# Performance work log

Measured on AMD Instinct MI355X. Metric: run time of the kernel, lower is better.

## Reference

```python
import jax, jax.numpy as jnp
import numpy as np

N = 50000      # nodes
E = 800000     # edges (avg degree 16)
H = 128        # hidden_nf
NORM_FACTOR = 100.0   # normalization_factor, aggregation 'sum'
NORM_CONST = 1.0      # norm_constant (effective_constant = max(1, 1.0))
EPS = 1e-8


def silu(v):
    return v * jax.nn.sigmoid(v)


def setup_inputs() -> dict:
    key = jax.random.key(0)
    ks = jax.random.split(key, 16)
    IN_E = 2 * H + 2  # edge MLP input: h[row] | h[col] | [radial, edge_attr]

    def w(k, shape, scale=0.05):
        return jax.random.normal(k, shape, dtype=jnp.float32) * scale

    return {
        "h": jax.random.normal(ks[0], (N, H), dtype=jnp.float32),
        "x": jax.random.normal(ks[1], (N, 3), dtype=jnp.float32),
        "edge_index": jax.random.randint(ks[2], (2, E), 0, N, dtype=jnp.int32),
        "edge_attr": jax.random.normal(ks[3], (E, 1), dtype=jnp.float32),
        "node_mask": jnp.ones((N, 1), dtype=jnp.float32),
        "edge_mask": jnp.ones((E, 1), dtype=jnp.float32),
        # 2 stacked GCL layers (identical shapes -> stacked on leading dim)
        "gcl_e_w1": w(ks[4], (2, IN_E, H)), "gcl_e_b1": jnp.zeros((2, H), jnp.float32),
        "gcl_e_w2": w(ks[5], (2, H, H)),    "gcl_e_b2": jnp.zeros((2, H), jnp.float32),
        "gcl_a_w":  w(ks[6], (2, H, 1)),    "gcl_a_b":  jnp.zeros((2, 1), jnp.float32),
        "gcl_n_w1": w(ks[7], (2, 2 * H, H)),"gcl_n_b1": jnp.zeros((2, H), jnp.float32),
        "gcl_n_w2": w(ks[8], (2, H, H)),    "gcl_n_b2": jnp.zeros((2, H), jnp.float32),
        # EquivariantUpdate coord MLP (last layer xavier gain 0.001 -> tiny, no bias)
        "c_w1": w(ks[9], (IN_E, H)), "c_b1": jnp.zeros((H,), jnp.float32),
        "c_w2": w(ks[10], (H, H)),   "c_b2": jnp.zeros((H,), jnp.float32),
        "c_w3": w(ks[11], (H, 1), 0.001),
    }


def reference(h, x, edge_index, edge_attr, node_mask, edge_mask,
              gcl_e_w1, gcl_e_b1, gcl_e_w2, gcl_e_b2, gcl_a_w, gcl_a_b,
              gcl_n_w1, gcl_n_b1, gcl_n_w2, gcl_n_b2,
              c_w1, c_b1, c_w2, c_b2, c_w3):
    row, col = edge_index[0], edge_index[1]
    n_nodes = h.shape[0]

    # coord2diff
    diff = x[row] - x[col]                                  # [E,3]
    radial = jnp.sum(diff * diff, axis=1, keepdims=True)    # [E,1]
    norm = jnp.sqrt(radial + EPS)
    coord_diff = diff / (norm + NORM_CONST)

    # edge_attr = cat([distances, edge_attr])  -> edge_feat_nf = 2
    ea = jnp.concatenate([radial, edge_attr], axis=1)       # [E,2]

    # n_layers=2 GCLs with attention
    for i in range(2):
        einp = jnp.concatenate([h[row], h[col], ea], axis=1)             # [E,258]
        mij = silu(silu(einp @ gcl_e_w1[i] + gcl_e_b1[i]) @ gcl_e_w2[i] + gcl_e_b2[i])
        att = jax.nn.sigmoid(mij @ gcl_a_w[i] + gcl_a_b[i])
        ef = mij * att * edge_mask                                       # [E,H]
        agg = jax.ops.segment_sum(ef, row, num_segments=n_nodes) / NORM_FACTOR
        ninp = jnp.concatenate([h, agg], axis=1)                         # [N,2H]
        h = h + (silu(ninp @ gcl_n_w1[i] + gcl_n_b1[i]) @ gcl_n_w2[i] + gcl_n_b2[i])
        h = h * node_mask

    # EquivariantUpdate (tanh=False, reflection_equiv=True -> no cross term)
    einp = jnp.concatenate([h[row], h[col], ea], axis=1)
    phi = silu(silu(einp @ c_w1 + c_b1) @ c_w2 + c_b2) @ c_w3            # [E,1]
    trans = coord_diff * phi * edge_mask                                 # [E,3]
    aggx = jax.ops.segment_sum(trans, row, num_segments=n_nodes) / NORM_FACTOR
    x = (x + aggx) * node_mask

    h = h * node_mask
    return (h, x)
```

## Files before the change

### kernel.cpp

```cpp
#include <hip/hip_runtime.h>
#include <hip/hip_bf16.h>
#include <math.h>
#include <string.h>

#define DEV __device__ __forceinline__

typedef __bf16 bf16;
typedef bf16 bf16x8 __attribute__((ext_vector_type(8)));
typedef bf16 bf16x2 __attribute__((ext_vector_type(2)));
typedef float f32x4 __attribute__((ext_vector_type(4)));
typedef unsigned int uint;

constexpr int N_NODES = 50000;
constexpr int N_EDGES = 800000;
constexpr int H = 128;
constexpr int NB_SCAN = (N_NODES + 255) / 256;

DEV float fsilu(float x) { return x / (1.f + __expf(-x)); }
DEV float fsigmoid(float x) { return 1.f / (1.f + __expf(-x)); }


__global__ void transpose_pad_kernel(bf16* __restrict__ dst, const float* __restrict__ src,
                                     int K, int Nf, int KP) {
    int idx = blockIdx.x * 256 + threadIdx.x;
    if (idx >= Nf * KP) return;
    int n = idx / KP, k = idx - n * KP;
    dst[idx] = (k < K) ? (bf16)src[k * Nf + n] : (bf16)0.f;
}

__global__ void h_init_kernel(const float* __restrict__ h, float* __restrict__ h_cur, int n) {
    int i = blockIdx.x * 256 + threadIdx.x;
    if (i < n) h_cur[i] = h[i];
}

__global__ void out_h_kernel(const float* __restrict__ h_cur, const float* __restrict__ nmask,
                             float* __restrict__ out) {
    int i = blockIdx.x * 256 + threadIdx.x;
    if (i < N_NODES * H) out[i] = h_cur[i] * nmask[i >> 7];
}


__global__ void count_kernel(const int* __restrict__ ei, int* __restrict__ deg) {
    int e = blockIdx.x * 256 + threadIdx.x;
    if (e < N_EDGES) atomicAdd(&deg[ei[e]], 1);
}

__global__ void scan1_kernel(const int* __restrict__ deg, int* __restrict__ off,
                             int* __restrict__ bsum) {
    __shared__ int s[256];
    int t = threadIdx.x, i = blockIdx.x * 256 + t;
    int v = (i < N_NODES) ? deg[i] : 0;
    s[t] = v;
    __syncthreads();
#pragma unroll
    for (int st = 1; st < 256; st <<= 1) {
        int x = (t >= st) ? s[t - st] : 0;
        __syncthreads();
        s[t] += x;
        __syncthreads();
    }
    if (i < N_NODES) off[i] = s[t] - v;
    if (t == 255) bsum[blockIdx.x] = s[255];
}

__global__ void scan2_kernel(int* __restrict__ bsum) {
    __shared__ int s[256];
    int t = threadIdx.x;
    int v = (t < NB_SCAN) ? bsum[t] : 0;
    s[t] = v;
    __syncthreads();
#pragma unroll
    for (int st = 1; st < 256; st <<= 1) {
        int x = (t >= st) ? s[t - st] : 0;
        __syncthreads();
        s[t] += x;
        __syncthreads();
    }
    if (t < NB_SCAN) bsum[t] = s[t] - v;
}

__global__ void scan3_kernel(int* __restrict__ off, const int* __restrict__ bsum) {
    int i = blockIdx.x * 256 + threadIdx.x;
    if (i >= N_NODES) return;
    off[i] += bsum[blockIdx.x];
}

__global__ void fill2_kernel(const int* __restrict__ ei, const float* __restrict__ eattr,
                             const float* __restrict__ emask, int* __restrict__ off,
                             uint* __restrict__ rc_pm, bf16* __restrict__ eaem_pm) {
    int e = blockIdx.x * 256 + threadIdx.x;
    if (e >= N_EDGES) return;
    int r = ei[e], c = ei[N_EDGES + e];
    int slot = atomicAdd(&off[r], 1);
    rc_pm[slot] = ((uint)r << 16) | (uint)c;
    eaem_pm[(size_t)slot * 2 + 0] = (bf16)eattr[e];
    eaem_pm[(size_t)slot * 2 + 1] = (bf16)emask[e];
}

__global__ __launch_bounds__(256, 2) void pq_kernel(
    const float* __restrict__ h_cur, const bf16* __restrict__ w1t,
    const float* __restrict__ b1, bf16* __restrict__ P, bf16* __restrict__ Q) {
    __shared__ __align__(16) bf16 hs[64 * 128];
    int t = threadIdx.x, lane = t & 63, wv = t >> 6;
    int lr = lane & 15, lg = lane >> 4;
    int nbase = blockIdx.x * 64;

    {
        int nl = t >> 2, q = t & 3;
        int node = nbase + nl;
        if (node < N_NODES) {
            const float4* hr = (const float4*)(h_cur + (size_t)node * H);
#pragma unroll
            for (int c = 0; c < 4; ++c) {
                float4 v0 = hr[q * 8 + c * 2];
                float4 v1 = hr[q * 8 + c * 2 + 1];
                bf16x8 o;
                o[0] = (bf16)v0.x; o[1] = (bf16)v0.y; o[2] = (bf16)v0.z; o[3] = (bf16)v0.w;
                o[4] = (bf16)v1.x; o[5] = (bf16)v1.y; o[6] = (bf16)v1.z; o[7] = (bf16)v1.w;
                int sl = (q * 4 + c) ^ (nl & 7);
                *(bf16x8*)(hs + nl * 128 + sl * 8) = o;
            }
        } else {
#pragma unroll
            for (int c = 0; c < 4; ++c) {
                int sl = (q * 4 + c) ^ (nl & 7);
                *(bf16x8*)(hs + nl * 128 + sl * 8) = (bf16x8)(bf16)0.f;
            }
        }
    }
    __syncthreads();

    f32x4 aP[4][2], aQ[4][2];
#pragma unroll
    for (int er = 0; er < 4; ++er)
#pragma unroll
        for (int j = 0; j < 2; ++j) { aP[er][j] = (f32x4)0.f; aQ[er][j] = (f32x4)0.f; }

    const bf16* bp0 = w1t + (size_t)((wv * 2 + 0) * 16 + lr) * 256 + lg * 8;
    const bf16* bp1 = w1t + (size_t)((wv * 2 + 1) * 16 + lr) * 256 + lg * 8;
#pragma unroll
    for (int kk = 0; kk < 4; ++kk) {
        bf16x8 a[4];
#pragma unroll
        for (int er = 0; er < 4; ++er) {
            int sl = (kk * 4 + lg) ^ (lr & 7);
            a[er] = *(const bf16x8*)(hs + (er * 16 + lr) * 128 + sl * 8);
        }
        bf16x8 bP0 = *(const bf16x8*)(bp0 + kk * 32);
        bf16x8 bP1 = *(const bf16x8*)(bp1 + kk * 32);
        bf16x8 bQ0 = *(const bf16x8*)(bp0 + 128 + kk * 32);
        bf16x8 bQ1 = *(const bf16x8*)(bp1 + 128 + kk * 32);
#pragma unroll
        for (int er = 0; er < 4; ++er) {
            aP[er][0] = __builtin_amdgcn_mfma_f32_16x16x32_bf16(a[er], bP0, aP[er][0], 0, 0, 0);
            aP[er][1] = __builtin_amdgcn_mfma_f32_16x16x32_bf16(a[er], bP1, aP[er][1], 0, 0, 0);
            aQ[er][0] = __builtin_amdgcn_mfma_f32_16x16x32_bf16(a[er], bQ0, aQ[er][0], 0, 0, 0);
            aQ[er][1] = __builtin_amdgcn_mfma_f32_16x16x32_bf16(a[er], bQ1, aQ[er][1], 0, 0, 0);
        }
    }

    float bb0 = b1[(wv * 2 + 0) * 16 + lr];
    float bb1v = b1[(wv * 2 + 1) * 16 + lr];
#pragma unroll
    for (int er = 0; er < 4; ++er) {
#pragma unroll
        for (int j = 0; j < 2; ++j) {
            int feat = (wv * 2 + j) * 16 + lr;
            float bb = j ? bb1v : bb0;
#pragma unroll
            for (int r = 0; r < 4; ++r) {
                int node = nbase + er * 16 + lg * 4 + r;
                if (node < N_NODES) {
                    P[(size_t)node * H + feat] = (bf16)(aP[er][j][r] + bb);
                    Q[(size_t)node * H + feat] = (bf16)(aQ[er][j][r]);
                }
            }
        }
    }
}


__global__ __launch_bounds__(256) void gather_h_kernel(
    const bf16* __restrict__ ef, const int* __restrict__ off, bf16* __restrict__ agg_bf) {
    int t = threadIdx.x, lane = t & 63, wv = t >> 6;
    int n = blockIdx.x * 4 + wv;
    if (n >= N_NODES) return;
    int st = (n == 0) ? 0 : off[n - 1];
    int dg = off[n] - st;
    const bf16* bp = ef + (size_t)st * H + lane * 2;
    float s0 = 0.f, s1 = 0.f;
    for (int k = 0; k < dg; ++k) {
        uint v = *(const uint*)(bp + (size_t)k * H);
        s0 += __uint_as_float(v << 16);
        s1 += __uint_as_float(v & 0xffff0000u);
    }
    bf16x2 o;
    o[0] = (bf16)(s0 * 0.01f);
    o[1] = (bf16)(s1 * 0.01f);
    *(bf16x2*)(agg_bf + (size_t)n * H + lane * 2) = o;
}

__global__ __launch_bounds__(256) void gather_x_kernel(
    const float* __restrict__ trans, const int* __restrict__ off,
    const float* __restrict__ x, const float* __restrict__ nmask, float* __restrict__ outx) {
    int t = threadIdx.x, lane = t & 63, wv = t >> 6;
    int n = blockIdx.x * 4 + wv;
    if (n >= N_NODES) return;
    int st = (n == 0) ? 0 : off[n - 1];
    int dg = off[n] - st;
    float sx = 0.f, sy = 0.f, sz = 0.f;
    for (int k = lane; k < dg; k += 64) {
        const float* tp = trans + (size_t)(st + k) * 3;
        sx += tp[0];
        sy += tp[1];
        sz += tp[2];
    }
#pragma unroll
    for (int m = 1; m < 64; m <<= 1) {
        sx += __shfl_xor(sx, m);
        sy += __shfl_xor(sy, m);
        sz += __shfl_xor(sz, m);
    }
    if (lane == 0) {
        float nm = nmask[n];
        outx[n * 3 + 0] = (x[n * 3 + 0] + sx * 0.01f) * nm;
        outx[n * 3 + 1] = (x[n * 3 + 1] + sy * 0.01f) * nm;
        outx[n * 3 + 2] = (x[n * 3 + 2] + sz * 0.01f) * nm;
    }
}


template <int KCHUNKS, int ASTRIDE, int BSTRIDE>
DEV void wave_gemm(const bf16* A_lds, const bf16* __restrict__ Bt,
                   f32x4 (&acc)[4][2], int lr, int lg, int wv) {
#pragma unroll
    for (int kk = 0; kk < KCHUNKS; ++kk) {
        int ko = kk * 32 + lg * 8;
        bf16x8 a[4], b[2];
#pragma unroll
        for (int er = 0; er < 4; ++er)
            a[er] = *(const bf16x8*)(A_lds + (er * 16 + lr) * ASTRIDE + ko);
#pragma unroll
        for (int j = 0; j < 2; ++j)
            b[j] = *(const bf16x8*)(Bt + (size_t)((wv * 2 + j) * 16 + lr) * BSTRIDE + ko);
#pragma unroll
        for (int er = 0; er < 4; ++er)
#pragma unroll
            for (int j = 0; j < 2; ++j)
                acc[er][j] = __builtin_amdgcn_mfma_f32_16x16x32_bf16(a[er], b[j], acc[er][j], 0, 0, 0);
    }
}

DEV void epi_silu_store(const f32x4 (&acc)[4][2], const float* __restrict__ bias,
                        bf16* out_lds, int OSTRIDE, int lr, int lg, int wv) {
    float b0 = bias[(wv * 2 + 0) * 16 + lr];
    float b1 = bias[(wv * 2 + 1) * 16 + lr];
#pragma unroll
    for (int er = 0; er < 4; ++er) {
#pragma unroll
        for (int j = 0; j < 2; ++j) {
            float bb = j ? b1 : b0;
            int fcol = (wv * 2 + j) * 16 + lr;
#pragma unroll
            for (int r = 0; r < 4; ++r) {
                int rrow = er * 16 + lg * 4 + r;
                out_lds[rrow * OSTRIDE + fcol] = (bf16)fsilu(acc[er][j][r] + bb);
            }
        }
    }
}

DEV void epi_silu_store_swz(const f32x4 (&acc)[4][2], const float* __restrict__ bias,
                            bf16* out_lds, int lr, int lg, int wv) {
    float b0 = bias[(wv * 2 + 0) * 16 + lr];
    float b1 = bias[(wv * 2 + 1) * 16 + lr];
#pragma unroll
    for (int er = 0; er < 4; ++er) {
#pragma unroll
        for (int j = 0; j < 2; ++j) {
            float bb = j ? b1 : b0;
            int fcol = (wv * 2 + j) * 16 + lr;
#pragma unroll
            for (int r = 0; r < 4; ++r) {
                int rrow = er * 16 + lg * 4 + r;
                int sl = (fcol >> 3) ^ (rrow & 7);
                out_lds[rrow * 128 + sl * 8 + (fcol & 7)] = (bf16)fsilu(acc[er][j][r] + bb);
            }
        }
    }
}

template <int MODE>
__global__ __launch_bounds__(256, 4) void edge_kernel(
    const bf16* __restrict__ P, const bf16* __restrict__ Q,
    const uint* __restrict__ rc_pm, const bf16* __restrict__ eaem_pm,
    const float* __restrict__ xg,
    const float* __restrict__ w_r, const float* __restrict__ w_e,
    const bf16* __restrict__ w2t, const float* __restrict__ b2,
    const float* __restrict__ avec, const float* __restrict__ abias,
    bf16* __restrict__ efout, float* __restrict__ trans) {
    __shared__ __align__(16) bf16 AR[64 * 128];
    __shared__ __align__(16) bf16 AC[64 * 128];
    __shared__ __align__(16) float avec_l[128];

    int t = threadIdx.x, lane = t & 63, wv = t >> 6;
    int lr = lane & 15, lg = lane >> 4;
    int ebase = blockIdx.x * 64;
    int el = t >> 2, q = t & 3;

    {
        int rsub = lane >> 4;
        int slot = lane & 15;
#pragma unroll
        for (int u = 0; u < 4; ++u) {
            int r = wv * 16 + u * 4 + rsub;
            uint rc = rc_pm[ebase + r];
            int nr = (int)(rc >> 16);
            int nc = (int)(rc & 0xffffu);
            int sl = slot ^ (r & 7);
            const bf16* gpr = P + (size_t)nr * H + sl * 8;
            __builtin_amdgcn_global_load_lds(
                (const __attribute__((address_space(1))) void*)gpr,
                (__attribute__((address_space(3))) void*)&AR[(wv * 16 + u * 4) * 128],
                16, 0, 0);
            const bf16* gpc = Q + (size_t)nc * H + sl * 8;
            __builtin_amdgcn_global_load_lds(
                (const __attribute__((address_space(1))) void*)gpc,
                (__attribute__((address_space(3))) void*)&AC[(wv * 16 + u * 4) * 128],
                16, 0, 0);
        }
    }
    if (t >= 64 && t < 192) avec_l[t - 64] = avec[t - 64];

    uint rc = rc_pm[ebase + el];
    int rr = (int)(rc >> 16), cc = (int)(rc & 0xffffu);
    float dx = xg[rr * 3 + 0] - xg[cc * 3 + 0];
    float dy = xg[rr * 3 + 1] - xg[cc * 3 + 1];
    float dz = xg[rr * 3 + 2] - xg[cc * 3 + 2];
    float radial = dx * dx + dy * dy + dz * dz;
    uint eu = *(const uint*)(eaem_pm + (size_t)(ebase + el) * 2);
    bf16x2 ep = __builtin_bit_cast(bf16x2, eu);
    float eattr = (float)ep[0];
    float em = (float)ep[1];

    __syncthreads();

#pragma unroll
    for (int c = 0; c < 4; ++c) {
        int sl = (q * 4 + c) ^ (el & 7);
        bf16* ap = AR + el * 128 + sl * 8;
        bf16x8 pv = *(const bf16x8*)ap;
        bf16x8 qv = *(const bf16x8*)(AC + el * 128 + sl * 8);
        f32x4 wr0 = *(const f32x4*)(w_r + q * 32 + c * 8);
        f32x4 wr1 = *(const f32x4*)(w_r + q * 32 + c * 8 + 4);
        f32x4 we0 = *(const f32x4*)(w_e + q * 32 + c * 8);
        f32x4 we1 = *(const f32x4*)(w_e + q * 32 + c * 8 + 4);
        bf16x8 o;
#pragma unroll
        for (int jj = 0; jj < 4; ++jj) {
            float v = (float)pv[jj] + (float)qv[jj] + radial * wr0[jj] + eattr * we0[jj];
            o[jj] = (bf16)fsilu(v);
        }
#pragma unroll
        for (int jj = 0; jj < 4; ++jj) {
            float v = (float)pv[4 + jj] + (float)qv[4 + jj] + radial * wr1[jj] + eattr * we1[jj];
            o[4 + jj] = (bf16)fsilu(v);
        }
        *(bf16x8*)ap = o;
    }
    __syncthreads();

    f32x4 acc2[4][2];
#pragma unroll
    for (int er = 0; er < 4; ++er)
#pragma unroll
        for (int j = 0; j < 2; ++j) acc2[er][j] = (f32x4)0.f;
    {
        const bf16* cp0 = w2t + (size_t)((wv * 2 + 0) * 16 + lr) * 128 + lg * 8;
        const bf16* cp1 = w2t + (size_t)((wv * 2 + 1) * 16 + lr) * 128 + lg * 8;
#pragma unroll
        for (int kk = 0; kk < 4; ++kk) {
            bf16x8 a[4], b[2];
            b[0] = *(const bf16x8*)(cp0 + kk * 32);
            b[1] = *(const bf16x8*)(cp1 + kk * 32);
#pragma unroll
            for (int er = 0; er < 4; ++er) {
                int sl = (kk * 4 + lg) ^ (lr & 7);
                a[er] = *(const bf16x8*)(AR + (er * 16 + lr) * 128 + sl * 8);
            }
#pragma unroll
            for (int er = 0; er < 4; ++er)
#pragma unroll
                for (int j = 0; j < 2; ++j)
                    acc2[er][j] = __builtin_amdgcn_mfma_f32_16x16x32_bf16(a[er], b[j], acc2[er][j], 0, 0, 0);
        }
    }

    epi_silu_store_swz(acc2, b2, AC, lr, lg, wv);
    __syncthreads();

    float part = 0.f;
    bf16x8 mv[4];
#pragma unroll
    for (int c = 0; c < 4; ++c) {
        int sl = (q * 4 + c) ^ (el & 7);
        mv[c] = *(const bf16x8*)(AC + el * 128 + sl * 8);
        f32x4 av0 = *(const f32x4*)(avec_l + q * 32 + c * 8);
        f32x4 av1 = *(const f32x4*)(avec_l + q * 32 + c * 8 + 4);
#pragma unroll
        for (int jj = 0; jj < 4; ++jj) part += (float)mv[c][jj] * av0[jj];
#pragma unroll
        for (int jj = 0; jj < 4; ++jj) part += (float)mv[c][4 + jj] * av1[jj];
    }
    part += __shfl_xor(part, 1);
    part += __shfl_xor(part, 2);

    if (MODE == 0) {
        float att = fsigmoid(part + abias[0]);
        float scale = att * em;
        bf16* edst = efout + (size_t)(ebase + el) * H + q * 32;
#pragma unroll
        for (int c = 0; c < 4; ++c) {
            bf16x8 o;
#pragma unroll
            for (int jj = 0; jj < 8; ++jj) o[jj] = (bf16)((float)mv[c][jj] * scale);
            *(bf16x8*)(edst + c * 8) = o;
        }
    } else {
        if (q == 0) {
            float inv = 1.f / (sqrtf(radial + 1e-8f) + 1.f);
            float s = part * em * inv;
            int sI = ebase + el;
            trans[sI * 3 + 0] = dx * s;
            trans[sI * 3 + 1] = dy * s;
            trans[sI * 3 + 2] = dz * s;
        }
    }
}

__global__ __launch_bounds__(256, 2) void node_kernel(
    float* __restrict__ h_cur, const bf16* __restrict__ agg_bf,
    const bf16* __restrict__ w1t, const float* __restrict__ b1,
    const bf16* __restrict__ w2t, const float* __restrict__ b2,
    const float* __restrict__ nmask) {
    constexpr int SRN = 264;
    constexpr int TRN = 136;
    __shared__ __align__(16) bf16 ninp[64 * SRN];
    __shared__ __align__(16) bf16 t1[64 * TRN];

    int t = threadIdx.x, lane = t & 63, wv = t >> 6;
    int lr = lane & 15, lg = lane >> 4;
    int nbase = blockIdx.x * 64;

    {
        int nl = t >> 2, q = t & 3;
        int node = nbase + nl;
        bf16* dst = ninp + nl * SRN;
        if (node < N_NODES) {
            const float4* hr = (const float4*)(h_cur + (size_t)node * H);
            const bf16* ar = agg_bf + (size_t)node * H;
#pragma unroll
            for (int pp = 0; pp < 8; ++pp) {
                int ch = pp * 4 + q;
                float4 v = hr[ch];
                dst[ch * 4 + 0] = (bf16)v.x; dst[ch * 4 + 1] = (bf16)v.y;
                dst[ch * 4 + 2] = (bf16)v.z; dst[ch * 4 + 3] = (bf16)v.w;
            }
#pragma unroll
            for (int pp = 0; pp < 4; ++pp) {
                int ch = pp * 4 + q;
                *(bf16x8*)(dst + 128 + ch * 8) = *(const bf16x8*)(ar + ch * 8);
            }
        } else {
#pragma unroll
            for (int pp = 0; pp < 8; ++pp) {
                int ch = pp * 4 + q;
#pragma unroll
                for (int k = 0; k < 4; ++k) {
                    dst[ch * 4 + k] = (bf16)0.f;
                    dst[128 + ch * 4 + k] = (bf16)0.f;
                }
            }
        }
    }
    __syncthreads();

    f32x4 acc[4][2];
#pragma unroll
    for (int er = 0; er < 4; ++er)
#pragma unroll
        for (int j = 0; j < 2; ++j) acc[er][j] = (f32x4)0.f;
    wave_gemm<8, SRN, 256>(ninp, w1t, acc, lr, lg, wv);
    epi_silu_store(acc, b1, t1, TRN, lr, lg, wv);
    __syncthreads();

    f32x4 acc2[4][2];
#pragma unroll
    for (int er = 0; er < 4; ++er)
#pragma unroll
        for (int j = 0; j < 2; ++j) acc2[er][j] = (f32x4)0.f;
    wave_gemm<4, TRN, 128>(t1, w2t, acc2, lr, lg, wv);

    float bb0 = b2[(wv * 2 + 0) * 16 + lr];
    float bb1 = b2[(wv * 2 + 1) * 16 + lr];
#pragma unroll
    for (int er = 0; er < 4; ++er) {
#pragma unroll
        for (int j = 0; j < 2; ++j) {
            float bb = j ? bb1 : bb0;
            int feat = (wv * 2 + j) * 16 + lr;
#pragma unroll
            for (int r = 0; r < 4; ++r) {
                int node = nbase + er * 16 + lg * 4 + r;
                if (node < N_NODES) {
                    size_t idx = (size_t)node * H + feat;
                    float nm = nmask[node];
                    h_cur[idx] = (h_cur[idx] + acc2[er][j][r] + bb) * nm;
                }
            }
        }
    }
}

extern "C" void kernel_launch(void* const* d_in, const int* in_sizes, int n_in,
                              void* d_out, int out_size, void* d_ws, size_t ws_size,
                              hipStream_t stream) {
    (void)in_sizes; (void)n_in; (void)out_size; (void)ws_size;
    const float* h_in  = (const float*)d_in[0];
    const float* x_in  = (const float*)d_in[1];
    const int*   ei    = (const int*)d_in[2];
    const float* eattr = (const float*)d_in[3];
    const float* nmask = (const float*)d_in[4];
    const float* emask = (const float*)d_in[5];
    const float* e_w1  = (const float*)d_in[6];
    const float* e_b1  = (const float*)d_in[7];
    const float* e_w2  = (const float*)d_in[8];
    const float* e_b2  = (const float*)d_in[9];
    const float* a_w   = (const float*)d_in[10];
    const float* a_b   = (const float*)d_in[11];
    const float* n_w1  = (const float*)d_in[12];
    const float* n_b1  = (const float*)d_in[13];
    const float* n_w2  = (const float*)d_in[14];
    const float* n_b2  = (const float*)d_in[15];
    const float* c_w1  = (const float*)d_in[16];
    const float* c_b1  = (const float*)d_in[17];
    const float* c_w2  = (const float*)d_in[18];
    const float* c_b2  = (const float*)d_in[19];
    const float* c_w3  = (const float*)d_in[20];
    float* out = (float*)d_out;

    char* p = (char*)d_ws;
    auto alloc = [&](size_t bytes) { char* r = p; p += (bytes + 255) & ~(size_t)255; return r; };
    float* h_cur  = (float*)alloc((size_t)N_NODES * H * 4);
    bf16*  Pb     = (bf16*) alloc((size_t)N_NODES * H * 2);
    bf16*  Qb     = (bf16*) alloc((size_t)N_NODES * H * 2);
    bf16*  agg_bf = Qb;
    bf16*  ef     = (bf16*) alloc((size_t)N_EDGES * H * 2);
    float* trans  = (float*)ef;
    int*   deg    = (int*)  alloc((size_t)N_NODES * 4);
    int*   off    = (int*)  alloc((size_t)N_NODES * 4);
    int*   bsum   = (int*)  alloc((size_t)NB_SCAN * 4);
    uint*  rc_pm  = (uint*) alloc((size_t)N_EDGES * 4);
    bf16*  eaem_pm= (bf16*) alloc((size_t)N_EDGES * 2 * 2);
    bf16*  e_w1t  = (bf16*) alloc((size_t)2 * 128 * 256 * 2);
    bf16*  e_w2t  = (bf16*) alloc((size_t)2 * 128 * 128 * 2);
    bf16*  n_w1t  = (bf16*) alloc((size_t)2 * 128 * 256 * 2);
    bf16*  n_w2t  = (bf16*) alloc((size_t)2 * 128 * 128 * 2);
    bf16*  c_w1t  = (bf16*) alloc((size_t)128 * 256 * 2);
    bf16*  c_w2t  = (bf16*) alloc((size_t)128 * 128 * 2);

    auto tp = [&](bf16* dst, const float* src, int K, int KP) {
        int tot = 128 * KP;
        transpose_pad_kernel<<<(tot + 255) / 256, 256, 0, stream>>>(dst, src, K, 128, KP);
    };
    tp(e_w1t, e_w1, 258, 256);               tp(e_w1t + 128 * 256, e_w1 + 258 * 128, 258, 256);
    tp(e_w2t, e_w2, 128, 128);               tp(e_w2t + 128 * 128, e_w2 + 128 * 128, 128, 128);
    tp(n_w1t, n_w1, 256, 256);               tp(n_w1t + 128 * 256, n_w1 + 256 * 128, 256, 256);
    tp(n_w2t, n_w2, 128, 128);               tp(n_w2t + 128 * 128, n_w2 + 128 * 128, 128, 128);
    tp(c_w1t, c_w1, 258, 256);
    tp(c_w2t, c_w2, 128, 128);

    h_init_kernel<<<(N_NODES * H + 255) / 256, 256, 0, stream>>>(h_in, h_cur, N_NODES * H);

    hipMemsetAsync(deg, 0, (size_t)N_NODES * 4, stream);
    count_kernel<<<(N_EDGES + 255) / 256, 256, 0, stream>>>(ei, deg);
    scan1_kernel<<<NB_SCAN, 256, 0, stream>>>(deg, off, bsum);
    scan2_kernel<<<1, 256, 0, stream>>>(bsum);
    scan3_kernel<<<NB_SCAN, 256, 0, stream>>>(off, bsum);
    fill2_kernel<<<(N_EDGES + 255) / 256, 256, 0, stream>>>(
        ei, eattr, emask, off, rc_pm, eaem_pm);

    int ngrid = (N_NODES + 3) / 4;
    int pqgrid = (N_NODES + 63) / 64;
    for (int i = 0; i < 2; ++i) {
        pq_kernel<<<pqgrid, 256, 0, stream>>>(
            h_cur, e_w1t + (size_t)i * 128 * 256, e_b1 + i * H, Pb, Qb);
        edge_kernel<0><<<N_EDGES / 64, 256, 0, stream>>>(
            Pb, Qb, rc_pm, eaem_pm, x_in,
            e_w1 + (size_t)i * 258 * 128 + 256 * 128,
            e_w1 + (size_t)i * 258 * 128 + 257 * 128,
            e_w2t + (size_t)i * 128 * 128, e_b2 + i * H,
            a_w + i * H, a_b + i, ef, nullptr);
        gather_h_kernel<<<ngrid, 256, 0, stream>>>(ef, off, agg_bf);
        node_kernel<<<(N_NODES + 63) / 64, 256, 0, stream>>>(
            h_cur, agg_bf,
            n_w1t + (size_t)i * 128 * 256, n_b1 + i * H,
            n_w2t + (size_t)i * 128 * 128, n_b2 + i * H, nmask);
    }
    pq_kernel<<<pqgrid, 256, 0, stream>>>(h_cur, c_w1t, c_b1, Pb, Qb);
    edge_kernel<1><<<N_EDGES / 64, 256, 0, stream>>>(
        Pb, Qb, rc_pm, eaem_pm, x_in,
        c_w1 + 256 * 128, c_w1 + 257 * 128,
        c_w2t, c_b2, c_w3, nullptr, nullptr, trans);
    gather_x_kernel<<<ngrid, 256, 0, stream>>>(trans, off, x_in, nmask,
                                               out + (size_t)N_NODES * H);

    out_h_kernel<<<(N_NODES * H + 255) / 256, 256, 0, stream>>>(h_cur, nmask, out);
}
```

Before: 984.6 us.

## Halve edge kernel LDS by loading row features directly into registers

The edge kernel now keeps a single 16KB LDS tile instead of two. Row-node features are loaded straight from global memory into registers per thread, and only column-node features go through global_load_lds. The w_r and w_e weights are staged in LDS, an extra barrier makes the tile safe to reuse for the second-layer output, and launch bounds rise to 8 blocks per CU. The aim is higher occupancy to hide gather latency, at the cost of an extra sync, uncoalesced per-thread row loads and tighter register limits that may cause spills.

```diff
diff --git a/kernel.cpp b/kernel.cpp
--- a/kernel.cpp
+++ b/kernel.cpp
@@ -291,7 +291,7 @@
 }
 
 template <int MODE>
-__global__ __launch_bounds__(256, 4) void edge_kernel(
+__global__ __launch_bounds__(256, 8) void edge_kernel(
     const bf16* __restrict__ P, const bf16* __restrict__ Q,
     const uint* __restrict__ rc_pm, const bf16* __restrict__ eaem_pm,
     const float* __restrict__ xg,
@@ -299,9 +299,10 @@
     const bf16* __restrict__ w2t, const float* __restrict__ b2,
     const float* __restrict__ avec, const float* __restrict__ abias,
     bf16* __restrict__ efout, float* __restrict__ trans) {
-    __shared__ __align__(16) bf16 AR[64 * 128];
-    __shared__ __align__(16) bf16 AC[64 * 128];
+    __shared__ __align__(16) bf16 T[64 * 128];
     __shared__ __align__(16) float avec_l[128];
+    __shared__ __align__(16) float wr_l[128];
+    __shared__ __align__(16) float we_l[128];
 
     int t = threadIdx.x, lane = t & 63, wv = t >> 6;
     int lr = lane & 15, lg = lane >> 4;
@@ -314,23 +315,22 @@
 #pragma unroll
         for (int u = 0; u < 4; ++u) {
             int r = wv * 16 + u * 4 + rsub;
-            uint rc = rc_pm[ebase + r];
-            int nr = (int)(rc >> 16);
-            int nc = (int)(rc & 0xffffu);
+            uint rcs = rc_pm[ebase + r];
+            int nc = (int)(rcs & 0xffffu);
             int sl = slot ^ (r & 7);
-            const bf16* gpr = P + (size_t)nr * H + sl * 8;
-            __builtin_amdgcn_global_load_lds(
-                (const __attribute__((address_space(1))) void*)gpr,
-                (__attribute__((address_space(3))) void*)&AR[(wv * 16 + u * 4) * 128],
-                16, 0, 0);
             const bf16* gpc = Q + (size_t)nc * H + sl * 8;
             __builtin_amdgcn_global_load_lds(
                 (const __attribute__((address_space(1))) void*)gpc,
-                (__attribute__((address_space(3))) void*)&AC[(wv * 16 + u * 4) * 128],
+                (__attribute__((address_space(3))) void*)&T[(wv * 16 + u * 4) * 128],
                 16, 0, 0);
         }
     }
-    if (t >= 64 && t < 192) avec_l[t - 64] = avec[t - 64];
+    if (t < 128) {
+        avec_l[t] = avec[t];
+    } else {
+        wr_l[t - 128] = w_r[t - 128];
+        we_l[t - 128] = w_e[t - 128];
+    }
 
     uint rc = rc_pm[ebase + el];
     int rr = (int)(rc >> 16), cc = (int)(rc & 0xffffu);
@@ -343,18 +343,23 @@
     float eattr = (float)ep[0];
     float em = (float)ep[1];
 
+    bf16x8 pvr[4];
+    const bf16* Pp = P + (size_t)rr * H + q * 32;
+#pragma unroll
+    for (int c = 0; c < 4; ++c) pvr[c] = *(const bf16x8*)(Pp + c * 8);
+
     __syncthreads();
 
 #pragma unroll
     for (int c = 0; c < 4; ++c) {
         int sl = (q * 4 + c) ^ (el & 7);
-        bf16* ap = AR + el * 128 + sl * 8;
-        bf16x8 pv = *(const bf16x8*)ap;
-        bf16x8 qv = *(const bf16x8*)(AC + el * 128 + sl * 8);
-        f32x4 wr0 = *(const f32x4*)(w_r + q * 32 + c * 8);
-        f32x4 wr1 = *(const f32x4*)(w_r + q * 32 + c * 8 + 4);
-        f32x4 we0 = *(const f32x4*)(w_e + q * 32 + c * 8);
-        f32x4 we1 = *(const f32x4*)(w_e + q * 32 + c * 8 + 4);
+        bf16* ap = T + el * 128 + sl * 8;
+        bf16x8 qv = *(const bf16x8*)ap;
+        bf16x8 pv = pvr[c];
+        f32x4 wr0 = *(const f32x4*)(wr_l + q * 32 + c * 8);
+        f32x4 wr1 = *(const f32x4*)(wr_l + q * 32 + c * 8 + 4);
+        f32x4 we0 = *(const f32x4*)(we_l + q * 32 + c * 8);
+        f32x4 we1 = *(const f32x4*)(we_l + q * 32 + c * 8 + 4);
         bf16x8 o;
 #pragma unroll
         for (int jj = 0; jj < 4; ++jj) {
@@ -386,7 +391,7 @@
 #pragma unroll
             for (int er = 0; er < 4; ++er) {
                 int sl = (kk * 4 + lg) ^ (lr & 7);
-                a[er] = *(const bf16x8*)(AR + (er * 16 + lr) * 128 + sl * 8);
+                a[er] = *(const bf16x8*)(T + (er * 16 + lr) * 128 + sl * 8);
             }
 #pragma unroll
             for (int er = 0; er < 4; ++er)
@@ -395,8 +400,9 @@
                     acc2[er][j] = __builtin_amdgcn_mfma_f32_16x16x32_bf16(a[er], b[j], acc2[er][j], 0, 0, 0);
         }
     }
-
-    epi_silu_store_swz(acc2, b2, AC, lr, lg, wv);
+    __syncthreads();
+
+    epi_silu_store_swz(acc2, b2, T, lr, lg, wv);
     __syncthreads();
 
     float part = 0.f;
@@ -404,7 +410,7 @@
 #pragma unroll
     for (int c = 0; c < 4; ++c) {
         int sl = (q * 4 + c) ^ (el & 7);
-        mv[c] = *(const bf16x8*)(AC + el * 128 + sl * 8);
+        mv[c] = *(const bf16x8*)(T + el * 128 + sl * 8);
         f32x4 av0 = *(const f32x4*)(avec_l + q * 32 + c * 8);
         f32x4 av1 = *(const f32x4*)(avec_l + q * 32 + c * 8 + 4);
 #pragma unroll
```

Measured after the change: 881.2 us. -10.5%, faster.
